# Kernel optimization log

Hardware: AMD Instinct MI355X
Metric: run time of the kernel (lower is better)

Reference implementation:

```python
import jax, jax.numpy as jnp
import numpy as np

B, D, C = 512, 512, 100000
U_M, L_M, U_A, L_A = 0.8, 0.45, 110.0, 10.0
LAMBDA_G, SCALE = 35.0, 64.0


def setup_inputs() -> dict:
    key = jax.random.key(0)
    k1, k2, k3, k4 = jax.random.split(key, 4)
    x = jax.random.normal(k1, (B, D), dtype=jnp.float32)
    # magnitudes in [l_a, u_a] as in MagFace
    x_norm = L_A + (U_A - L_A) * jax.random.uniform(k2, (B,), dtype=jnp.float32)
    labels = jax.random.randint(k3, (B,), 0, C, dtype=jnp.int64)
    weight = jax.random.normal(k4, (C, D), dtype=jnp.float32)
    return {"x": x, "x_norm": x_norm, "labels": labels, "weight": weight}


def _l2norm(a, axis=-1, eps=1e-12):
    return a / jnp.maximum(jnp.linalg.norm(a, axis=axis, keepdims=True), eps)


def reference(x, x_norm, labels, weight):
    # adaptive margin per sample, shape [B]
    margin = (U_M - L_M) / (U_A - L_A) * (x_norm - L_A) + L_M

    # cos_theta = normalize(x) @ normalize(W).T  -> [B, C]
    cos_theta = jnp.clip(_l2norm(x) @ _l2norm(weight).T, -1.0, 1.0)

    theta = jnp.arccos(cos_theta)
    valid = labels != -1  # [B]
    safe_labels = jnp.where(valid, labels, 0)
    # add margin at the target class (only for valid labels)
    add = jnp.where(valid, margin, 0.0)  # [B]
    theta = theta.at[jnp.arange(theta.shape[0]), safe_labels].add(add)

    logits = jnp.cos(theta) * SCALE  # [B, C]

    # cross-entropy, ignoring labels == -1
    lse = jax.nn.logsumexp(logits, axis=-1)  # [B]
    tgt = jnp.take_along_axis(logits, safe_labels[:, None], axis=-1)[:, 0]
    nll = jnp.where(valid, lse - tgt, 0.0)
    n_valid = jnp.maximum(jnp.sum(valid.astype(jnp.float32)), 1.0)
    ce = jnp.sum(nll) / n_valid

    # MagFace G-loss
    g_loss = jnp.mean(x_norm / (U_A * U_A) + 1.0 / x_norm)

    return ce + LAMBDA_G * g_loss
```

## Files before the change

### kernel.cpp

```cpp
#include <hip/hip_runtime.h>

typedef unsigned short u16;
typedef unsigned int u32;
typedef float f32x4 __attribute__((ext_vector_type(4)));
typedef short bf16x8 __attribute__((ext_vector_type(8)));

#define U_M 0.8f
#define L_M 0.45f
#define U_A 110.0f
#define L_A 10.0f
#define LAMBDA_G 35.0f
#define SCALEF 64.0f

__device__ __forceinline__ u16 f2bf(float f) {
  u32 u = __builtin_bit_cast(u32, f);
  u32 r = (u + 0x7fffu + ((u >> 16) & 1u)) >> 16;
  return (u16)r;
}

__device__ __forceinline__ u32 cvtpk(float lo, float hi) {
  u32 r;
  asm("v_cvt_pk_bf16_f32 %0, %1, %2" : "=v"(r) : "v"(lo), "v"(hi));
  return r;
}

__global__ void xnorm_kernel(const float* __restrict__ x, u16* __restrict__ xn, int K) {
  int row = blockIdx.x * 4 + (threadIdx.x >> 6);
  int l = threadIdx.x & 63;
  const float4* p = reinterpret_cast<const float4*>(x + (size_t)row * K) + l * 2;
  float4 a = p[0], b = p[1];
  float s = a.x*a.x + a.y*a.y + a.z*a.z + a.w*a.w
          + b.x*b.x + b.y*b.y + b.z*b.z + b.w*b.w;
  #pragma unroll
  for (int m = 32; m >= 1; m >>= 1) s += __shfl_xor(s, m);
  float inv = rsqrtf(fmaxf(s, 1e-24f));
  u32 q0 = (u32)f2bf(a.x*inv) | ((u32)f2bf(a.y*inv) << 16);
  u32 q1 = (u32)f2bf(a.z*inv) | ((u32)f2bf(a.w*inv) << 16);
  u32 q2 = (u32)f2bf(b.x*inv) | ((u32)f2bf(b.y*inv) << 16);
  u32 q3 = (u32)f2bf(b.z*inv) | ((u32)f2bf(b.w*inv) << 16);
  *reinterpret_cast<uint4*>(xn + (size_t)row * K + l * 8) = make_uint4(q0, q1, q2, q3);
}

__global__ void tgt_kernel(const float* __restrict__ x, const float* __restrict__ W,
                           const int* __restrict__ labels, float* __restrict__ tgtcos, int K) {
  int b = blockIdx.x;
  int l = threadIdx.x;
  int lab = labels[b];
  int labc = lab < 0 ? 0 : lab;
  const float4* px = reinterpret_cast<const float4*>(x + (size_t)b * K) + l * 2;
  const float4* pw = reinterpret_cast<const float4*>(W + (size_t)labc * K) + l * 2;
  float4 a0 = px[0], a1 = px[1], w0 = pw[0], w1 = pw[1];
  float dot = a0.x*w0.x + a0.y*w0.y + a0.z*w0.z + a0.w*w0.w
            + a1.x*w1.x + a1.y*w1.y + a1.z*w1.z + a1.w*w1.w;
  float sx = a0.x*a0.x + a0.y*a0.y + a0.z*a0.z + a0.w*a0.w
           + a1.x*a1.x + a1.y*a1.y + a1.z*a1.z + a1.w*a1.w;
  float sw = w0.x*w0.x + w0.y*w0.y + w0.z*w0.z + w0.w*w0.w
           + w1.x*w1.x + w1.y*w1.y + w1.z*w1.z + w1.w*w1.w;
  #pragma unroll
  for (int m = 32; m >= 1; m >>= 1) {
    dot += __shfl_xor(dot, m);
    sx  += __shfl_xor(sx, m);
    sw  += __shfl_xor(sw, m);
  }
  if (l == 0) {
    float cv = dot * rsqrtf(fmaxf(sx, 1e-24f)) * rsqrtf(fmaxf(sw, 1e-24f));
    tgtcos[b] = fminf(fmaxf(cv, -1.f), 1.f);
  }
}

__global__ __launch_bounds__(256, 2) void gemm_gl(
    const u16* __restrict__ xn, const float* __restrict__ W,
    const int* __restrict__ labels,
    float* __restrict__ partials, int C, int K, int M) {
  __shared__ u16 sA[128 * 64];
  __shared__ float sBf[128 * 64];
  __shared__ float bsum[2][128];
  __shared__ float sIw[128];
  __shared__ int slab[128];

  int nwg = gridDim.x;
  int id = blockIdx.x;
  int q = nwg >> 3, r = nwg & 7;
  int xcd = id & 7, pos = id >> 3;
  int wg = (xcd < r ? xcd * (q + 1) : r * (q + 1) + (xcd - r) * q) + pos;
  const int bm = wg & 3, bn = wg >> 2;

  const int t = threadIdx.x;
  const int l = t & 63, wid = t >> 6;
  const int wm = wid >> 1, wn_ = wid & 1;
  const int n0 = bn * 128;
  if (t < 128) slab[t] = labels[bm * 128 + t];

  float ssq[4] = {0.f, 0.f, 0.f, 0.f};
  f32x4 acc[4][4] = {};
  const int nkt = K >> 6;

  for (int kt = 0; kt < nkt; ++kt) {
    const int k0 = kt << 6;

    #pragma unroll
    for (int i = 0; i < 4; ++i) {
      int L = i * 256 + t;
      int rr = L >> 3;
      int cs = (L & 7) ^ (rr & 7);
      const u16* src = xn + (size_t)(bm * 128 + rr) * K + k0 + cs * 8;
      __builtin_amdgcn_global_load_lds(
          (const __attribute__((address_space(1))) void*)src,
          (__attribute__((address_space(3))) void*)(sA + (size_t)(i * 256 + (t & 192)) * 8),
          16, 0, 0);
    }
    #pragma unroll
    for (int j = 0; j < 8; ++j) {
      int L = j * 256 + t;
      int rr = L >> 4;
      int cs = (L & 15) ^ (rr & 7);
      int gr = n0 + rr; gr = gr < C ? gr : C - 1;
      const float* src = W + (size_t)gr * K + k0 + cs * 4;
      __builtin_amdgcn_global_load_lds(
          (const __attribute__((address_space(1))) void*)src,
          (__attribute__((address_space(3))) void*)(sBf + (size_t)(j * 256 + (t & 192)) * 4),
          16, 0, 0);
    }

    __syncthreads();

    #pragma unroll
    for (int ks = 0; ks < 2; ++ks) {
      bf16x8 af[4], bfr[4];
      #pragma unroll
      for (int mi = 0; mi < 4; ++mi) {
        int row = wm * 64 + mi * 16 + (l & 15);
        int ch = ks * 4 + (l >> 4);
        af[mi] = *reinterpret_cast<const bf16x8*>(sA + row * 64 + ((ch ^ (row & 7)) * 8));
      }
      #pragma unroll
      for (int ni = 0; ni < 4; ++ni) {
        int row = wn_ * 64 + ni * 16 + (l & 15);
        int ch = ks * 4 + (l >> 4);
        int c1 = (2 * ch)     ^ (row & 7);
        int c2 = (2 * ch + 1) ^ (row & 7);
        f32x4 fa = *reinterpret_cast<const f32x4*>(sBf + row * 64 + c1 * 4);
        f32x4 fb = *reinterpret_cast<const f32x4*>(sBf + row * 64 + c2 * 4);
        if (wm == 0) {
          ssq[ni] += fa[0]*fa[0] + fa[1]*fa[1] + fa[2]*fa[2] + fa[3]*fa[3]
                   + fb[0]*fb[0] + fb[1]*fb[1] + fb[2]*fb[2] + fb[3]*fb[3];
        }
        uint4 u = make_uint4(cvtpk(fa[0], fa[1]), cvtpk(fa[2], fa[3]),
                             cvtpk(fb[0], fb[1]), cvtpk(fb[2], fb[3]));
        bfr[ni] = __builtin_bit_cast(bf16x8, u);
      }
      #pragma unroll
      for (int mi = 0; mi < 4; ++mi)
        #pragma unroll
        for (int ni = 0; ni < 4; ++ni)
          acc[mi][ni] = __builtin_amdgcn_mfma_f32_16x16x32_bf16(af[mi], bfr[ni], acc[mi][ni], 0, 0, 0);
    }
    __syncthreads();
  }

  if (wm == 0) {
    #pragma unroll
    for (int ni = 0; ni < 4; ++ni) {
      float s = ssq[ni];
      s += __shfl_xor(s, 16);
      s += __shfl_xor(s, 32);
      if ((l >> 4) == 0) sIw[wn_ * 64 + ni * 16 + l] = rsqrtf(fmaxf(s, 1e-24f));
    }
  }
  __syncthreads();

  float iw[4]; int colv[4];
  #pragma unroll
  for (int ni = 0; ni < 4; ++ni) {
    int cl = wn_ * 64 + ni * 16 + (l & 15);
    colv[ni] = n0 + cl;
    iw[ni] = sIw[cl];
  }
  #pragma unroll
  for (int mi = 0; mi < 4; ++mi) {
    #pragma unroll
    for (int rg = 0; rg < 4; ++rg) {
      int row_l = wm * 64 + mi * 16 + ((l >> 4) << 2) + rg;
      int labr = slab[row_l];
      float rs = 0.f;
      #pragma unroll
      for (int ni = 0; ni < 4; ++ni) {
        float cv = acc[mi][ni][rg] * iw[ni];
        cv = fminf(fmaxf(cv, -1.f), 1.f);
        float e = __expf(SCALEF * cv - SCALEF);
        bool keep = (colv[ni] < C) && (colv[ni] != labr);
        rs += keep ? e : 0.f;
      }
      rs += __shfl_xor(rs, 1);
      rs += __shfl_xor(rs, 2);
      rs += __shfl_xor(rs, 4);
      rs += __shfl_xor(rs, 8);
      if ((l & 15) == 0) bsum[wn_][row_l] = rs;
    }
  }
  __syncthreads();
  if (t < 128) {
    partials[(size_t)bn * M + bm * 128 + t] = bsum[0][t] + bsum[1][t];
  }
}

__global__ void rowreduce_kernel(const float* __restrict__ partials, float* __restrict__ rowsum,
                                 int NBN, int M) {
  int b = blockIdx.x, t = threadIdx.x;
  float s = 0.f;
  for (int i = t; i < NBN; i += 256) s += partials[(size_t)i * M + b];
  __shared__ float sh[256];
  sh[t] = s; __syncthreads();
  for (int off = 128; off >= 1; off >>= 1) {
    if (t < off) sh[t] += sh[t + off];
    __syncthreads();
  }
  if (t == 0) rowsum[b] = sh[0];
}

__global__ void final_kernel(const float* __restrict__ rowsum, const float* __restrict__ tgtcos,
                             const float* __restrict__ x_norm, const int* __restrict__ labels,
                             float* __restrict__ out, int Bn) {
  int t = threadIdx.x;
  float nll = 0.f, g = 0.f, vld = 0.f;
  if (t < Bn) {
    float a = x_norm[t];
    g = a * (1.0f / (U_A * U_A)) + 1.0f / a;
    int lab = labels[t];
    bool valid = (lab != -1);
    if (valid) {
      float ct = tgtcos[t];
      float margin = ((U_M - L_M) / (U_A - L_A)) * (a - L_A) + L_M;
      float theta = acosf(ct) + margin;
      float tl = SCALEF * cosf(theta);
      float se = rowsum[t] + __expf(tl - SCALEF);
      float lse = SCALEF + logf(se);
      nll = lse - tl;
      vld = 1.f;
    }
  }
  __shared__ float s1[512], s2[512], s3[512];
  s1[t] = nll; s2[t] = g; s3[t] = vld;
  __syncthreads();
  for (int off = 256; off >= 1; off >>= 1) {
    if (t < off) { s1[t] += s1[t + off]; s2[t] += s2[t + off]; s3[t] += s3[t + off]; }
    __syncthreads();
  }
  if (t == 0) {
    float ce = s1[0] / fmaxf(s3[0], 1.f);
    out[0] = ce + LAMBDA_G * (s2[0] / (float)Bn);
  }
}

extern "C" void kernel_launch(void* const* d_in, const int* in_sizes, int n_in,
                              void* d_out, int out_size, void* d_ws, size_t ws_size,
                              hipStream_t stream) {
  const float* x      = (const float*)d_in[0];
  const float* x_norm = (const float*)d_in[1];
  const int*   labels = (const int*)d_in[2];
  const float* W      = (const float*)d_in[3];
  float* out = (float*)d_out;

  const int B = in_sizes[1];
  const int D = in_sizes[0] / B;
  const int C = in_sizes[3] / D;
  const int NBN = (C + 127) / 128;

  char* ws = (char*)d_ws;
  size_t o_xn   = 0;
  size_t o_tgt  = o_xn + (size_t)B * D * 2;
  size_t o_rows = o_tgt + (size_t)B * 4;
  size_t o_part = o_rows + (size_t)B * 4;

  u16*   xn       = (u16*)(ws + o_xn);
  float* tgtcos   = (float*)(ws + o_tgt);
  float* rowsum   = (float*)(ws + o_rows);
  float* partials = (float*)(ws + o_part);

  hipLaunchKernelGGL(xnorm_kernel, dim3(B / 4), dim3(256), 0, stream, x, xn, D);
  hipLaunchKernelGGL(tgt_kernel, dim3(B), dim3(64), 0, stream, x, W, labels, tgtcos, D);
  hipLaunchKernelGGL(gemm_gl, dim3(NBN * (B / 128)), dim3(256), 0, stream,
                     xn, W, labels, partials, C, D, B);
  hipLaunchKernelGGL(rowreduce_kernel, dim3(B), dim3(256), 0, stream, partials, rowsum, NBN, B);
  hipLaunchKernelGGL(final_kernel, dim3(1), dim3(B), 0, stream, rowsum, tgtcos, x_norm, labels, out, B);
}
```

Measured before the change: 121.7 us.

## Double-buffer W tiles in LDS with async prefetch and split row partials

The GEMM keeps two LDS buffers for the fp32 weight tile. It prefetches the next K-slice of W with global_load_lds while the current slice is converted to bf16 and fed to MFMAs, and it uses explicit vmcnt waits and raw barriers in place of __syncthreads. The aim is to hide global-memory latency when streaming the large weight matrix. The final per-block shared-memory reduction is dropped: each wave half writes its own row partial straight to global memory, and rowreduce sums twice as many slots. LDS use per block rises to 80 KB, which may limit occupancy, and the partials buffer doubles in size.

```diff
diff --git a/kernel.cpp b/kernel.cpp
--- a/kernel.cpp
+++ b/kernel.cpp
@@ -68,15 +68,16 @@
   }
 }
 
-__global__ __launch_bounds__(256, 2) void gemm_gl(
+__global__ __launch_bounds__(256, 2) void gemm_cnt(
     const u16* __restrict__ xn, const float* __restrict__ W,
     const int* __restrict__ labels,
     float* __restrict__ partials, int C, int K, int M) {
-  __shared__ u16 sA[128 * 64];
-  __shared__ float sBf[128 * 64];
-  __shared__ float bsum[2][128];
-  __shared__ float sIw[128];
-  __shared__ int slab[128];
+  __shared__ __align__(16) char smem[81920];
+  u16*   sA  = (u16*)smem;
+  float* sB0 = (float*)(smem + 16384);
+  float* sB1 = (float*)(smem + 49152);
+  float* sIw  = (float*)(smem);
+  int*   slab = (int*)(smem + 512);
 
   int nwg = gridDim.x;
   int id = blockIdx.x;
@@ -89,14 +90,32 @@
   const int l = t & 63, wid = t >> 6;
   const int wm = wid >> 1, wn_ = wid & 1;
   const int n0 = bn * 128;
-  if (t < 128) slab[t] = labels[bm * 128 + t];
 
   float ssq[4] = {0.f, 0.f, 0.f, 0.f};
   f32x4 acc[4][4] = {};
   const int nkt = K >> 6;
 
+  #pragma unroll
+  for (int j = 0; j < 8; ++j) {
+    int L = j * 256 + t;
+    int rr = L >> 4;
+    int cs = (L & 15) ^ (rr & 7);
+    int gr = n0 + rr; gr = gr < C ? gr : C - 1;
+    const float* src = W + (size_t)gr * K + cs * 4;
+    __builtin_amdgcn_global_load_lds(
+        (const __attribute__((address_space(1))) void*)src,
+        (__attribute__((address_space(3))) void*)(sB0 + (size_t)(j * 256 + (t & 192)) * 4),
+        16, 0, 0);
+  }
+
   for (int kt = 0; kt < nkt; ++kt) {
     const int k0 = kt << 6;
+    const bool pf = (kt + 1) < nkt;
+    const float* bCur = (kt & 1) ? sB1 : sB0;
+    float* bNxt = (kt & 1) ? sB0 : sB1;
+
+    asm volatile("s_waitcnt vmcnt(0)" ::: "memory");
+    __builtin_amdgcn_s_barrier();
 
     #pragma unroll
     for (int i = 0; i < 4; ++i) {
@@ -109,54 +128,66 @@
           (__attribute__((address_space(3))) void*)(sA + (size_t)(i * 256 + (t & 192)) * 8),
           16, 0, 0);
     }
-    #pragma unroll
-    for (int j = 0; j < 8; ++j) {
-      int L = j * 256 + t;
-      int rr = L >> 4;
-      int cs = (L & 15) ^ (rr & 7);
-      int gr = n0 + rr; gr = gr < C ? gr : C - 1;
-      const float* src = W + (size_t)gr * K + k0 + cs * 4;
-      __builtin_amdgcn_global_load_lds(
-          (const __attribute__((address_space(1))) void*)src,
-          (__attribute__((address_space(3))) void*)(sBf + (size_t)(j * 256 + (t & 192)) * 4),
-          16, 0, 0);
-    }
-
-    __syncthreads();
-
+    if (pf) {
+      const int k1 = (kt + 1) << 6;
+      #pragma unroll
+      for (int j = 0; j < 8; ++j) {
+        int L = j * 256 + t;
+        int rr = L >> 4;
+        int cs = (L & 15) ^ (rr & 7);
+        int gr = n0 + rr; gr = gr < C ? gr : C - 1;
+        const float* src = W + (size_t)gr * K + k1 + cs * 4;
+        __builtin_amdgcn_global_load_lds(
+            (const __attribute__((address_space(1))) void*)src,
+            (__attribute__((address_space(3))) void*)(bNxt + (size_t)(j * 256 + (t & 192)) * 4),
+            16, 0, 0);
+      }
+    }
+
+    bf16x8 bfr[2][4];
     #pragma unroll
     for (int ks = 0; ks < 2; ++ks) {
-      bf16x8 af[4], bfr[4];
-      #pragma unroll
-      for (int mi = 0; mi < 4; ++mi) {
-        int row = wm * 64 + mi * 16 + (l & 15);
-        int ch = ks * 4 + (l >> 4);
-        af[mi] = *reinterpret_cast<const bf16x8*>(sA + row * 64 + ((ch ^ (row & 7)) * 8));
-      }
       #pragma unroll
       for (int ni = 0; ni < 4; ++ni) {
         int row = wn_ * 64 + ni * 16 + (l & 15);
         int ch = ks * 4 + (l >> 4);
         int c1 = (2 * ch)     ^ (row & 7);
         int c2 = (2 * ch + 1) ^ (row & 7);
-        f32x4 fa = *reinterpret_cast<const f32x4*>(sBf + row * 64 + c1 * 4);
-        f32x4 fb = *reinterpret_cast<const f32x4*>(sBf + row * 64 + c2 * 4);
+        f32x4 fa = *reinterpret_cast<const f32x4*>(bCur + row * 64 + c1 * 4);
+        f32x4 fb = *reinterpret_cast<const f32x4*>(bCur + row * 64 + c2 * 4);
         if (wm == 0) {
           ssq[ni] += fa[0]*fa[0] + fa[1]*fa[1] + fa[2]*fa[2] + fa[3]*fa[3]
                    + fb[0]*fb[0] + fb[1]*fb[1] + fb[2]*fb[2] + fb[3]*fb[3];
         }
         uint4 u = make_uint4(cvtpk(fa[0], fa[1]), cvtpk(fa[2], fa[3]),
                              cvtpk(fb[0], fb[1]), cvtpk(fb[2], fb[3]));
-        bfr[ni] = __builtin_bit_cast(bf16x8, u);
+        bfr[ks][ni] = __builtin_bit_cast(bf16x8, u);
+      }
+    }
+
+    if (pf) asm volatile("s_waitcnt vmcnt(8)" ::: "memory");
+    else    asm volatile("s_waitcnt vmcnt(0)" ::: "memory");
+    __builtin_amdgcn_s_barrier();
+    __builtin_amdgcn_sched_barrier(0);
+
+    #pragma unroll
+    for (int ks = 0; ks < 2; ++ks) {
+      bf16x8 af[4];
+      #pragma unroll
+      for (int mi = 0; mi < 4; ++mi) {
+        int row = wm * 64 + mi * 16 + (l & 15);
+        int ch = ks * 4 + (l >> 4);
+        af[mi] = *reinterpret_cast<const bf16x8*>(sA + row * 64 + ((ch ^ (row & 7)) * 8));
       }
       #pragma unroll
       for (int mi = 0; mi < 4; ++mi)
         #pragma unroll
         for (int ni = 0; ni < 4; ++ni)
-          acc[mi][ni] = __builtin_amdgcn_mfma_f32_16x16x32_bf16(af[mi], bfr[ni], acc[mi][ni], 0, 0, 0);
-    }
-    __syncthreads();
-  }
+          acc[mi][ni] = __builtin_amdgcn_mfma_f32_16x16x32_bf16(af[mi], bfr[ks][ni], acc[mi][ni], 0, 0, 0);
+    }
+  }
+
+  __syncthreads();
 
   if (wm == 0) {
     #pragma unroll
@@ -167,6 +198,7 @@
       if ((l >> 4) == 0) sIw[wn_ * 64 + ni * 16 + l] = rsqrtf(fmaxf(s, 1e-24f));
     }
   }
+  if (t < 128) slab[t] = labels[bm * 128 + t];
   __syncthreads();
 
   float iw[4]; int colv[4];
@@ -195,20 +227,17 @@
       rs += __shfl_xor(rs, 2);
       rs += __shfl_xor(rs, 4);
       rs += __shfl_xor(rs, 8);
-      if ((l & 15) == 0) bsum[wn_][row_l] = rs;
-    }
-  }
-  __syncthreads();
-  if (t < 128) {
-    partials[(size_t)bn * M + bm * 128 + t] = bsum[0][t] + bsum[1][t];
+      if ((l & 15) == 0)
+        partials[((size_t)bn * 2 + wn_) * M + bm * 128 + row_l] = rs;
+    }
   }
 }
 
 __global__ void rowreduce_kernel(const float* __restrict__ partials, float* __restrict__ rowsum,
-                                 int NBN, int M) {
+                                 int NSLOT, int M) {
   int b = blockIdx.x, t = threadIdx.x;
   float s = 0.f;
-  for (int i = t; i < NBN; i += 256) s += partials[(size_t)i * M + b];
+  for (int i = t; i < NSLOT; i += 256) s += partials[(size_t)i * M + b];
   __shared__ float sh[256];
   sh[t] = s; __syncthreads();
   for (int off = 128; off >= 1; off >>= 1) {
@@ -279,8 +308,8 @@
 
   hipLaunchKernelGGL(xnorm_kernel, dim3(B / 4), dim3(256), 0, stream, x, xn, D);
   hipLaunchKernelGGL(tgt_kernel, dim3(B), dim3(64), 0, stream, x, W, labels, tgtcos, D);
-  hipLaunchKernelGGL(gemm_gl, dim3(NBN * (B / 128)), dim3(256), 0, stream,
+  hipLaunchKernelGGL(gemm_cnt, dim3(NBN * (B / 128)), dim3(256), 0, stream,
                      xn, W, labels, partials, C, D, B);
-  hipLaunchKernelGGL(rowreduce_kernel, dim3(B), dim3(256), 0, stream, partials, rowsum, NBN, B);
+  hipLaunchKernelGGL(rowreduce_kernel, dim3(B), dim3(256), 0, stream, partials, rowsum, NBN * 2, B);
   hipLaunchKernelGGL(final_kernel, dim3(1), dim3(B), 0, stream, rowsum, tgtcos, x_norm, labels, out, B);
 }
```

Result: slower. 141.8 us (+16.5%).

## Pre-normalize W to bf16 in a separate kernel before the GEMM

Applied to the files above, without the earlier changes.

Adds a wprep kernel that L2-normalizes each weight row and stores it as bf16 in the workspace. The GEMM then loads bf16 W tiles directly, which removes the in-loop fp32-to-bf16 conversion, the sum-of-squares accumulation and the inverse-norm epilogue. Halving the B-tile shared memory also allows raising the launch bounds to 4 blocks per CU. The cost is an extra full pass over fp32 W plus a bf16 write and re-read, which adds HBM traffic to a workload that is already bandwidth-heavy.

```diff
diff --git a/kernel.cpp b/kernel.cpp
--- a/kernel.cpp
+++ b/kernel.cpp
@@ -16,12 +16,6 @@
   u32 u = __builtin_bit_cast(u32, f);
   u32 r = (u + 0x7fffu + ((u >> 16) & 1u)) >> 16;
   return (u16)r;
-}
-
-__device__ __forceinline__ u32 cvtpk(float lo, float hi) {
-  u32 r;
-  asm("v_cvt_pk_bf16_f32 %0, %1, %2" : "=v"(r) : "v"(lo), "v"(hi));
-  return r;
 }
 
 __global__ void xnorm_kernel(const float* __restrict__ x, u16* __restrict__ xn, int K) {
@@ -39,6 +33,23 @@
   u32 q2 = (u32)f2bf(b.x*inv) | ((u32)f2bf(b.y*inv) << 16);
   u32 q3 = (u32)f2bf(b.z*inv) | ((u32)f2bf(b.w*inv) << 16);
   *reinterpret_cast<uint4*>(xn + (size_t)row * K + l * 8) = make_uint4(q0, q1, q2, q3);
+}
+
+__global__ void wprep_kernel(const float* __restrict__ W, u16* __restrict__ wn, int K) {
+  int row = blockIdx.x * 4 + (threadIdx.x >> 6);
+  int l = threadIdx.x & 63;
+  const float4* p = reinterpret_cast<const float4*>(W + (size_t)row * K) + l * 2;
+  float4 a = p[0], b = p[1];
+  float s = a.x*a.x + a.y*a.y + a.z*a.z + a.w*a.w
+          + b.x*b.x + b.y*b.y + b.z*b.z + b.w*b.w;
+  #pragma unroll
+  for (int m = 32; m >= 1; m >>= 1) s += __shfl_xor(s, m);
+  float inv = rsqrtf(fmaxf(s, 1e-24f));
+  u32 q0 = (u32)f2bf(a.x*inv) | ((u32)f2bf(a.y*inv) << 16);
+  u32 q1 = (u32)f2bf(a.z*inv) | ((u32)f2bf(a.w*inv) << 16);
+  u32 q2 = (u32)f2bf(b.x*inv) | ((u32)f2bf(b.y*inv) << 16);
+  u32 q3 = (u32)f2bf(b.z*inv) | ((u32)f2bf(b.w*inv) << 16);
+  *reinterpret_cast<uint4*>(wn + (size_t)row * K + l * 8) = make_uint4(q0, q1, q2, q3);
 }
 
 __global__ void tgt_kernel(const float* __restrict__ x, const float* __restrict__ W,
@@ -68,14 +79,13 @@
   }
 }
 
-__global__ __launch_bounds__(256, 2) void gemm_gl(
-    const u16* __restrict__ xn, const float* __restrict__ W,
+__global__ __launch_bounds__(256, 4) void gemm_bf16(
+    const u16* __restrict__ xn, const u16* __restrict__ wn,
     const int* __restrict__ labels,
     float* __restrict__ partials, int C, int K, int M) {
   __shared__ u16 sA[128 * 64];
-  __shared__ float sBf[128 * 64];
+  __shared__ u16 sB[128 * 64];
   __shared__ float bsum[2][128];
-  __shared__ float sIw[128];
   __shared__ int slab[128];
 
   int nwg = gridDim.x;
@@ -91,13 +101,10 @@
   const int n0 = bn * 128;
   if (t < 128) slab[t] = labels[bm * 128 + t];
 
-  float ssq[4] = {0.f, 0.f, 0.f, 0.f};
   f32x4 acc[4][4] = {};
   const int nkt = K >> 6;
-
   for (int kt = 0; kt < nkt; ++kt) {
     const int k0 = kt << 6;
-
     #pragma unroll
     for (int i = 0; i < 4; ++i) {
       int L = i * 256 + t;
@@ -110,20 +117,18 @@
           16, 0, 0);
     }
     #pragma unroll
-    for (int j = 0; j < 8; ++j) {
-      int L = j * 256 + t;
-      int rr = L >> 4;
-      int cs = (L & 15) ^ (rr & 7);
-      int gr = n0 + rr; gr = gr < C ? gr : C - 1;
-      const float* src = W + (size_t)gr * K + k0 + cs * 4;
+    for (int i = 0; i < 4; ++i) {
+      int L = i * 256 + t;
+      int rr = L >> 3;
+      int cs = (L & 7) ^ (rr & 7);
+      int grow = n0 + rr; grow = grow < C ? grow : C - 1;
+      const u16* src = wn + (size_t)grow * K + k0 + cs * 8;
       __builtin_amdgcn_global_load_lds(
           (const __attribute__((address_space(1))) void*)src,
-          (__attribute__((address_space(3))) void*)(sBf + (size_t)(j * 256 + (t & 192)) * 4),
+          (__attribute__((address_space(3))) void*)(sB + (size_t)(i * 256 + (t & 192)) * 8),
           16, 0, 0);
     }
-
-    __syncthreads();
-
+    __syncthreads();
     #pragma unroll
     for (int ks = 0; ks < 2; ++ks) {
       bf16x8 af[4], bfr[4];
@@ -137,17 +142,7 @@
       for (int ni = 0; ni < 4; ++ni) {
         int row = wn_ * 64 + ni * 16 + (l & 15);
         int ch = ks * 4 + (l >> 4);
-        int c1 = (2 * ch)     ^ (row & 7);
-        int c2 = (2 * ch + 1) ^ (row & 7);
-        f32x4 fa = *reinterpret_cast<const f32x4*>(sBf + row * 64 + c1 * 4);
-        f32x4 fb = *reinterpret_cast<const f32x4*>(sBf + row * 64 + c2 * 4);
-        if (wm == 0) {
-          ssq[ni] += fa[0]*fa[0] + fa[1]*fa[1] + fa[2]*fa[2] + fa[3]*fa[3]
-                   + fb[0]*fb[0] + fb[1]*fb[1] + fb[2]*fb[2] + fb[3]*fb[3];
-        }
-        uint4 u = make_uint4(cvtpk(fa[0], fa[1]), cvtpk(fa[2], fa[3]),
-                             cvtpk(fb[0], fb[1]), cvtpk(fb[2], fb[3]));
-        bfr[ni] = __builtin_bit_cast(bf16x8, u);
+        bfr[ni] = *reinterpret_cast<const bf16x8*>(sB + row * 64 + ((ch ^ (row & 7)) * 8));
       }
       #pragma unroll
       for (int mi = 0; mi < 4; ++mi)
@@ -157,25 +152,9 @@
     }
     __syncthreads();
   }
-
-  if (wm == 0) {
-    #pragma unroll
-    for (int ni = 0; ni < 4; ++ni) {
-      float s = ssq[ni];
-      s += __shfl_xor(s, 16);
-      s += __shfl_xor(s, 32);
-      if ((l >> 4) == 0) sIw[wn_ * 64 + ni * 16 + l] = rsqrtf(fmaxf(s, 1e-24f));
-    }
-  }
-  __syncthreads();
-
-  float iw[4]; int colv[4];
-  #pragma unroll
-  for (int ni = 0; ni < 4; ++ni) {
-    int cl = wn_ * 64 + ni * 16 + (l & 15);
-    colv[ni] = n0 + cl;
-    iw[ni] = sIw[cl];
-  }
+  int colv[4];
+  #pragma unroll
+  for (int ni = 0; ni < 4; ++ni) colv[ni] = n0 + wn_ * 64 + ni * 16 + (l & 15);
   #pragma unroll
   for (int mi = 0; mi < 4; ++mi) {
     #pragma unroll
@@ -185,7 +164,7 @@
       float rs = 0.f;
       #pragma unroll
       for (int ni = 0; ni < 4; ++ni) {
-        float cv = acc[mi][ni][rg] * iw[ni];
+        float cv = acc[mi][ni][rg];
         cv = fminf(fmaxf(cv, -1.f), 1.f);
         float e = __expf(SCALEF * cv - SCALEF);
         bool keep = (colv[ni] < C) && (colv[ni] != labr);
@@ -271,16 +250,19 @@
   size_t o_tgt  = o_xn + (size_t)B * D * 2;
   size_t o_rows = o_tgt + (size_t)B * 4;
   size_t o_part = o_rows + (size_t)B * 4;
+  size_t o_wn   = o_part + (size_t)NBN * B * 4;
 
   u16*   xn       = (u16*)(ws + o_xn);
   float* tgtcos   = (float*)(ws + o_tgt);
   float* rowsum   = (float*)(ws + o_rows);
   float* partials = (float*)(ws + o_part);
+  u16*   wn       = (u16*)(ws + o_wn);
 
   hipLaunchKernelGGL(xnorm_kernel, dim3(B / 4), dim3(256), 0, stream, x, xn, D);
   hipLaunchKernelGGL(tgt_kernel, dim3(B), dim3(64), 0, stream, x, W, labels, tgtcos, D);
-  hipLaunchKernelGGL(gemm_gl, dim3(NBN * (B / 128)), dim3(256), 0, stream,
-                     xn, W, labels, partials, C, D, B);
+  hipLaunchKernelGGL(wprep_kernel, dim3(C / 4), dim3(256), 0, stream, W, wn, D);
+  hipLaunchKernelGGL(gemm_bf16, dim3(NBN * (B / 128)), dim3(256), 0, stream,
+                     xn, wn, labels, partials, C, D, B);
   hipLaunchKernelGGL(rowreduce_kernel, dim3(B), dim3(256), 0, stream, partials, rowsum, NBN, B);
   hipLaunchKernelGGL(final_kernel, dim3(1), dim3(B), 0, stream, rowsum, tgtcos, x_norm, labels, out, B);
 }
```

After: 131.2 us. +7.9%, slower.
